# Optimization experiments

Measured on AMD Instinct MI355X. Metric: run time of the kernel, lower is better.

## Reference

```python
import jax, jax.numpy as jnp
import numpy as np

NUM_NODES = 100000
NUM_EDGES = 1600000
IN_DIM, HID_DIM, OUT_DIM = 128, 128, 70


def gcn_conv(x, edge_index, W, b):
    """PyG-style GCNConv: linear transform, add self-loops, symmetric
    degree-normalized scatter-add aggregation, plus bias."""
    n = x.shape[0]
    xw = x @ W  # [N, D_out]
    src, dst = edge_index[0], edge_index[1]  # messages flow src -> dst
    loop = jnp.arange(n)
    src = jnp.concatenate([src, loop])
    dst = jnp.concatenate([dst, loop])
    # degree computed at target nodes (with self-loops), edge weight 1
    deg = jax.ops.segment_sum(jnp.ones_like(dst, dtype=xw.dtype), dst,
                              num_segments=n)
    dinv = jnp.where(deg > 0, jax.lax.rsqrt(deg), 0.0)
    norm = dinv[src] * dinv[dst]  # [E+N]
    msgs = xw[src] * norm[:, None]  # [E+N, D_out] gathered messages
    out = jax.ops.segment_sum(msgs, dst, num_segments=n)
    return out + b


def setup_inputs() -> dict:
    key = jax.random.key(0)
    k = jax.random.split(key, 6)
    x = jax.random.normal(k[0], (NUM_NODES, IN_DIM), dtype=jnp.float32)
    edge_index = jax.random.randint(k[1], (2, NUM_EDGES), 0, NUM_NODES,
                                    dtype=jnp.int64)
    # Glorot-style init for weights, zero bias (PyG default)
    W1 = jax.random.normal(k[2], (IN_DIM, HID_DIM), dtype=jnp.float32) / np.sqrt(IN_DIM)
    b1 = jnp.zeros((HID_DIM,), dtype=jnp.float32)
    W2 = jax.random.normal(k[3], (HID_DIM, OUT_DIM), dtype=jnp.float32) / np.sqrt(HID_DIM)
    b2 = jnp.zeros((OUT_DIM,), dtype=jnp.float32)
    return {"x": x, "edge_index": edge_index, "W1": W1, "b1": b1,
            "W2": W2, "b2": b2}


def reference(x, edge_index, W1, b1, W2, b2):
    h = gcn_conv(x, edge_index, W1, b1)
    h = jax.nn.relu(h)
    # dropout(p=0.5) is identity in eval mode
    out = gcn_conv(h, edge_index, W2, b2)
    return out
```

## Files before the change

### kernel.cpp

```cpp
#include <hip/hip_runtime.h>
#include <hip/hip_bf16.h>


#define BSH 8
#define BCHUNK 4096
#define BCAP 8192

typedef __attribute__((ext_vector_type(8))) short short8;
typedef __attribute__((ext_vector_type(4))) float float4v;
typedef __attribute__((ext_vector_type(2))) float float2v;

__device__ __forceinline__ float bf_lo(unsigned u) { return __uint_as_float(u << 16); }
__device__ __forceinline__ float bf_hi(unsigned u) { return __uint_as_float(u & 0xffff0000u); }
__device__ __forceinline__ float bf2f(unsigned short h) {
    return __uint_as_float((unsigned)h << 16);
}
__device__ __forceinline__ unsigned short f2bf(float f) {
    unsigned u = __float_as_uint(f);
    u += 0x7fff + ((u >> 16) & 1);
    return (unsigned short)(u >> 16);
}
__device__ __forceinline__ void acc8(float* acc, uint4 m) {
    acc[0] += bf_lo(m.x); acc[1] += bf_hi(m.x);
    acc[2] += bf_lo(m.y); acc[3] += bf_hi(m.y);
    acc[4] += bf_lo(m.z); acc[5] += bf_hi(m.z);
    acc[6] += bf_lo(m.w); acc[7] += bf_hi(m.w);
}

__global__ __launch_bounds__(512) void k_bucket_scatter(
        const int* __restrict__ src, const int* __restrict__ dst,
        int* __restrict__ bwcur, unsigned long long* __restrict__ tmp, int E, int nb) {
    __shared__ int lh[512];
    __shared__ int lb[512];
    int t = threadIdx.x;
    for (int j = t; j < nb; j += 512) lh[j] = 0;
    __syncthreads();
    int e0 = blockIdx.x * BCHUNK;
    int e1 = min(E, e0 + BCHUNK);
    for (int e = e0 + t; e < e1; e += 512) atomicAdd(&lh[dst[e] >> BSH], 1);
    __syncthreads();
    for (int j = t; j < nb; j += 512) {
        int c = lh[j];
        lb[j] = c ? atomicAdd(&bwcur[j], c) : 0;
        lh[j] = 0;
    }
    __syncthreads();
    for (int e = e0 + t; e < e1; e += 512) {
        int d = dst[e];
        int b = d >> BSH;
        int o = atomicAdd(&lh[b], 1);
        int pos = lb[b] + o;
        if (pos < BCAP)
            tmp[(size_t)b * BCAP + pos] =
                ((unsigned long long)(unsigned)d << 32) | (unsigned)src[e];
    }
}

__global__ __launch_bounds__(512) void k_bucket_finalize(
        const unsigned long long* __restrict__ tmp, const int* __restrict__ bwcur,
        int* __restrict__ deg, float* __restrict__ dinv,
        int* __restrict__ rs, int* __restrict__ csr, int N) {
    __shared__ int cnt[256];
    __shared__ int sc[256];
    int b = blockIdx.x;
    int t = threadIdx.x;
    int e0 = b * BCAP;
    int e1 = e0 + min(bwcur[b], BCAP);
    if (t < 256) cnt[t] = 0;
    __syncthreads();
    for (int e = e0 + t; e < e1; e += 512) {
        int d = (int)(tmp[e] >> 32);
        atomicAdd(&cnt[d & 255], 1);
    }
    __syncthreads();
    int c = (t < 256) ? cnt[t] : 0;
    if (t < 256) sc[t] = c;
    __syncthreads();
    for (int off = 1; off < 256; off <<= 1) {
        int add = (t >= off && t < 256) ? sc[t - off] : 0;
        __syncthreads();
        if (t < 256) sc[t] += add;
        __syncthreads();
    }
    int excl = (t < 256) ? (sc[t] - c) : 0;
    __syncthreads();
    if (t < 256) sc[t] = excl;
    int node = (b << BSH) + t;
    if (t < 256 && node < N) {
        deg[node] = c;
        dinv[node] = rsqrtf((float)(c + 1));
        rs[node] = e0 + excl;
    }
    if (t < 256) cnt[t] = 0;
    __syncthreads();
    for (int e = e0 + t; e < e1; e += 512) {
        unsigned long long p = tmp[e];
        int j = ((int)(p >> 32)) & 255;
        int o = atomicAdd(&cnt[j], 1);
        csr[e0 + sc[j] + o] = (int)(p & 0xffffffffu);
    }
}

__global__ void k_prep_w(const float* __restrict__ W1, const float* __restrict__ W2,
                         unsigned short* __restrict__ w1th, unsigned short* __restrict__ w1tl,
                         unsigned short* __restrict__ w2th, unsigned short* __restrict__ w2tl,
                         int* __restrict__ bwcur) {
    if (blockIdx.x >= 104) {
        int idx = (blockIdx.x - 104) * 256 + threadIdx.x;
        if (idx < 512) bwcur[idx] = 0;
        return;
    }
    int i = blockIdx.x * blockDim.x + threadIdx.x;
    if (i < 128 * 128) {
        int col = i % 128, k = i / 128;
        float w = W1[k * 128 + col];
        unsigned short h = f2bf(w);
        w1th[(size_t)col * 128 + k] = h;
        w1tl[(size_t)col * 128 + k] = f2bf(w - bf2f(h));
    } else if (i < 128 * 128 + 80 * 128) {
        int j = i - 128 * 128;
        int col = j % 80, k = j / 80;
        float w = (col < 70) ? W2[k * 70 + col] : 0.f;
        unsigned short h = f2bf(w);
        w2th[(size_t)col * 128 + k] = h;
        w2tl[(size_t)col * 128 + k] = f2bf(w - bf2f(h));
    }
}

template <int DOUT, int OSTRIDE, int NT>
__global__ __launch_bounds__(256, 3) void k_gemm_mfma(
        const float* __restrict__ X, const unsigned short* __restrict__ Wth,
        const unsigned short* __restrict__ Wtl,
        const float* __restrict__ dinv, unsigned short* __restrict__ Y, int n) {
    __shared__ short xs_h[64][136];
    __shared__ short xs_l[64][136];
    int t = threadIdx.x;
    int lane = t & 63, wave = t >> 6;
    int m16 = lane & 15, quad = lane >> 4;
    int r0 = blockIdx.x * 64;

    short8 bh[2][4], bl[2][4];
    int nt0 = wave, nt1 = wave + 4;
#pragma unroll
    for (int i = 0; i < 2; i++) {
        int nt = i ? nt1 : nt0;
        if (nt >= NT) continue;
        int col = nt * 16 + m16;
#pragma unroll
        for (int kc = 0; kc < 4; kc++) {
            bh[i][kc] = *(const short8*)&Wth[(size_t)col * 128 + kc * 32 + quad * 8];
            bl[i][kc] = *(const short8*)&Wtl[(size_t)col * 128 + kc * 32 + quad * 8];
        }
    }

    for (int p = t; p < 64 * 32; p += 256) {
        int row = p >> 5;
        int k4 = p & 31;
        int gr = r0 + row;
        if (gr >= n) gr = n - 1;
        float4v xv = __builtin_nontemporal_load(
            (const float4v*)(X + (size_t)gr * 128 + 4 * k4));
        unsigned short h0 = f2bf(xv.x), h1 = f2bf(xv.y);
        unsigned short h2 = f2bf(xv.z), h3 = f2bf(xv.w);
        unsigned short l0 = f2bf(xv.x - bf2f(h0)), l1 = f2bf(xv.y - bf2f(h1));
        unsigned short l2 = f2bf(xv.z - bf2f(h2)), l3 = f2bf(xv.w - bf2f(h3));
        *(uint2*)&xs_h[row][4 * k4] =
            make_uint2((unsigned)h0 | ((unsigned)h1 << 16), (unsigned)h2 | ((unsigned)h3 << 16));
        *(uint2*)&xs_l[row][4 * k4] =
            make_uint2((unsigned)l0 | ((unsigned)l1 << 16), (unsigned)l2 | ((unsigned)l3 << 16));
    }
    __syncthreads();

    float4v acc[2][4];
#pragma unroll
    for (int i = 0; i < 2; i++)
#pragma unroll
        for (int ms = 0; ms < 4; ms++) acc[i][ms] = (float4v){0.f, 0.f, 0.f, 0.f};

#pragma unroll
    for (int kc = 0; kc < 4; kc++) {
#pragma unroll
        for (int ms = 0; ms < 4; ms++) {
            short8 ah = *(short8*)&xs_h[ms * 16 + m16][kc * 32 + quad * 8];
            short8 al = *(short8*)&xs_l[ms * 16 + m16][kc * 32 + quad * 8];
#pragma unroll
            for (int i = 0; i < 2; i++) {
                int nt = i ? nt1 : nt0;
                if (nt >= NT) continue;
                acc[i][ms] = __builtin_amdgcn_mfma_f32_16x16x32_bf16(ah, bh[i][kc], acc[i][ms], 0, 0, 0);
                acc[i][ms] = __builtin_amdgcn_mfma_f32_16x16x32_bf16(al, bh[i][kc], acc[i][ms], 0, 0, 0);
                acc[i][ms] = __builtin_amdgcn_mfma_f32_16x16x32_bf16(ah, bl[i][kc], acc[i][ms], 0, 0, 0);
            }
        }
    }

#pragma unroll
    for (int i = 0; i < 2; i++) {
        int nt = i ? nt1 : nt0;
        if (nt >= NT) continue;
        int col = nt * 16 + m16;
        if (col >= OSTRIDE) continue;
#pragma unroll
        for (int ms = 0; ms < 4; ms++) {
#pragma unroll
            for (int r = 0; r < 4; r++) {
                int row = r0 + ms * 16 + quad * 4 + r;
                if (row < n) {
                    float val = (col < DOUT) ? acc[i][ms][r] * dinv[row] : 0.f;
                    Y[(size_t)row * OSTRIDE + col] = f2bf(val);
                }
            }
        }
    }
}

__global__ __launch_bounds__(256, 8) void k_agg_w128(
        const uint4* __restrict__ msg, const float* __restrict__ dinv,
        const int* __restrict__ rs, const int* __restrict__ deg,
        const int* __restrict__ csr, const float* __restrict__ bias,
        float* __restrict__ out, int n) {
    int lane = threadIdx.x & 63;
    int q = lane & 15;
    int slot = lane >> 4;
    int wid = blockIdx.x * 4 + (threadIdx.x >> 6);
    int nw = gridDim.x * 4;
    for (int v = wid; v < n; v += nw) {
        int start = rs[v];
        int cnt = deg[v];
        float dv = dinv[v];
        uint4 mself = msg[(size_t)v * 16 + q];
        float acc[8] = {0.f, 0.f, 0.f, 0.f, 0.f, 0.f, 0.f, 0.f};
        int i = slot;
        for (; i + 12 < cnt; i += 16) {
            int s0 = csr[start + i];
            int s1 = csr[start + i + 4];
            int s2 = csr[start + i + 8];
            int s3 = csr[start + i + 12];
            uint4 m0 = msg[(size_t)s0 * 16 + q];
            uint4 m1 = msg[(size_t)s1 * 16 + q];
            uint4 m2 = msg[(size_t)s2 * 16 + q];
            uint4 m3 = msg[(size_t)s3 * 16 + q];
            acc8(acc, m0);
            acc8(acc, m1);
            acc8(acc, m2);
            acc8(acc, m3);
        }
        for (; i + 4 < cnt; i += 8) {
            int s0 = csr[start + i];
            int s1 = csr[start + i + 4];
            uint4 m0 = msg[(size_t)s0 * 16 + q];
            uint4 m1 = msg[(size_t)s1 * 16 + q];
            acc8(acc, m0);
            acc8(acc, m1);
        }
        if (i < cnt) {
            int s = csr[start + i];
            uint4 m = msg[(size_t)s * 16 + q];
            acc8(acc, m);
        }
#pragma unroll
        for (int j = 0; j < 8; j++) acc[j] += __shfl_xor(acc[j], 32);
#pragma unroll
        for (int j = 0; j < 8; j++) acc[j] += __shfl_xor(acc[j], 16);
        if (slot == 0) {
            float o[8];
            o[0] = acc[0] + bf_lo(mself.x); o[1] = acc[1] + bf_hi(mself.x);
            o[2] = acc[2] + bf_lo(mself.y); o[3] = acc[3] + bf_hi(mself.y);
            o[4] = acc[4] + bf_lo(mself.z); o[5] = acc[5] + bf_hi(mself.z);
            o[6] = acc[6] + bf_lo(mself.w); o[7] = acc[7] + bf_hi(mself.w);
            float r[8];
#pragma unroll
            for (int j = 0; j < 8; j++) r[j] = fmaxf(dv * o[j] + bias[8 * q + j], 0.f);
            float4v* op = (float4v*)(out + (size_t)v * 128 + 8 * q);
            __builtin_nontemporal_store((float4v){r[0], r[1], r[2], r[3]}, op);
            __builtin_nontemporal_store((float4v){r[4], r[5], r[6], r[7]}, op + 1);
        }
    }
}

__global__ __launch_bounds__(256, 8) void k_agg_w72(
        const uint4* __restrict__ msg, const float* __restrict__ dinv,
        const int* __restrict__ rs, const int* __restrict__ deg,
        const int* __restrict__ csr, const float* __restrict__ bias,
        float* __restrict__ out, int n) {
    int lane = threadIdx.x & 63;
    int slot = lane / 9;
    int q = lane - slot * 9;
    bool active = lane < 63;
    int wid = blockIdx.x * 4 + (threadIdx.x >> 6);
    int nw = gridDim.x * 4;
    for (int v = wid; v < n; v += nw) {
        int start = rs[v];
        int cnt = deg[v];
        float dv = dinv[v];
        float acc[8] = {0.f, 0.f, 0.f, 0.f, 0.f, 0.f, 0.f, 0.f};
        uint4 mself = make_uint4(0, 0, 0, 0);
        if (active) {
            mself = msg[(size_t)v * 9 + q];
            int i = slot;
            for (; i + 14 < cnt; i += 21) {
                int s0 = csr[start + i];
                int s1 = csr[start + i + 7];
                int s2 = csr[start + i + 14];
                uint4 m0 = msg[(size_t)s0 * 9 + q];
                uint4 m1 = msg[(size_t)s1 * 9 + q];
                uint4 m2 = msg[(size_t)s2 * 9 + q];
                acc8(acc, m0);
                acc8(acc, m1);
                acc8(acc, m2);
            }
            for (; i + 7 < cnt; i += 14) {
                int s0 = csr[start + i];
                int s1 = csr[start + i + 7];
                uint4 m0 = msg[(size_t)s0 * 9 + q];
                uint4 m1 = msg[(size_t)s1 * 9 + q];
                acc8(acc, m0);
                acc8(acc, m1);
            }
            if (i < cnt) {
                int s = csr[start + i];
                uint4 m = msg[(size_t)s * 9 + q];
                acc8(acc, m);
            }
        }
#pragma unroll
        for (int j = 0; j < 8; j++) {
            float t27 = __shfl(acc[j], lane + 27);
            if (lane < 27) acc[j] += t27;
        }
#pragma unroll
        for (int j = 0; j < 8; j++) {
            float t54 = __shfl(acc[j], lane + 54);
            float t9  = __shfl(acc[j], lane + 9);
            float t18 = __shfl(acc[j], lane + 18);
            if (lane < 9) acc[j] += t54 + t9 + t18;
        }
        if (lane < 9) {
            float o[8];
            o[0] = acc[0] + bf_lo(mself.x); o[1] = acc[1] + bf_hi(mself.x);
            o[2] = acc[2] + bf_lo(mself.y); o[3] = acc[3] + bf_hi(mself.y);
            o[4] = acc[4] + bf_lo(mself.z); o[5] = acc[5] + bf_hi(mself.z);
            o[6] = acc[6] + bf_lo(mself.w); o[7] = acc[7] + bf_hi(mself.w);
            float* orow = out + (size_t)v * 70 + 8 * q;
#pragma unroll
            for (int jj = 0; jj < 4; jj++) {
                int f = 8 * q + 2 * jj;
                if (f < 70) {
                    float2 st = make_float2(dv * o[2 * jj] + bias[f],
                                            dv * o[2 * jj + 1] + bias[f + 1]);
                    *(float2*)(orow + 2 * jj) = st;
                }
            }
        }
    }
}

static inline size_t alignup(size_t x) { return (x + 255) & ~(size_t)255; }

extern "C" void kernel_launch(void* const* d_in, const int* in_sizes, int n_in,
                              void* d_out, int out_size, void* d_ws, size_t ws_size,
                              hipStream_t stream) {
    const float* x = (const float*)d_in[0];
    const int* edge = (const int*)d_in[1];
    const float* W1 = (const float*)d_in[2];
    const float* b1 = (const float*)d_in[3];
    const float* W2 = (const float*)d_in[4];
    const float* b2 = (const float*)d_in[5];

    const int N = in_sizes[0] / 128;
    const int E = in_sizes[1] / 2;
    const int* src = edge;
    const int* dst = edge + E;
    const int nb = (N + 255) >> BSH;

    char* w = (char*)d_ws;
    int* deg = (int*)w;              w += alignup((size_t)N * 4);
    float* dinv = (float*)w;         w += alignup((size_t)N * 4);
    int* rs = (int*)w;               w += alignup((size_t)N * 4);
    int* bwcur = (int*)w;            w += alignup(4096);
    int* csr = (int*)w;              w += alignup((size_t)nb * BCAP * 4);
    unsigned short* msg1 = (unsigned short*)w; w += alignup((size_t)N * 128 * 2);
    unsigned short* msg2 = (unsigned short*)w; w += alignup((size_t)N * 72 * 2);
    unsigned short* w1th = (unsigned short*)w; w += alignup(128 * 128 * 2);
    unsigned short* w1tl = (unsigned short*)w; w += alignup(128 * 128 * 2);
    unsigned short* w2th = (unsigned short*)w; w += alignup(80 * 128 * 2);
    unsigned short* w2tl = (unsigned short*)w; w += alignup(80 * 128 * 2);
    float* h = (float*)w;            w += alignup((size_t)N * 128 * 4);
    unsigned long long* tmp = (unsigned long long*)h;

    k_prep_w<<<104 + 2, 256, 0, stream>>>(W1, W2, w1th, w1tl, w2th, w2tl, bwcur);

    k_bucket_scatter<<<(E + BCHUNK - 1) / BCHUNK, 512, 0, stream>>>(src, dst, bwcur, tmp, E, nb);
    k_bucket_finalize<<<nb, 512, 0, stream>>>(tmp, bwcur, deg, dinv, rs, csr, N);

    int gblocks = (N + 63) / 64;

    k_gemm_mfma<128, 128, 8><<<gblocks, 256, 0, stream>>>(x, w1th, w1tl, dinv, msg1, N);
    k_agg_w128<<<2048, 256, 0, stream>>>((const uint4*)msg1, dinv, rs, deg, csr, b1, h, N);

    k_gemm_mfma<70, 72, 5><<<gblocks, 256, 0, stream>>>(h, w2th, w2tl, dinv, msg2, N);
    k_agg_w72<<<2048, 256, 0, stream>>>((const uint4*)msg2, dinv, rs, deg, csr, b2,
                                        (float*)d_out, N);
}
```

Before: 329.1 us.

## Split layer-2 messages into 64-wide main and 8-wide tail arrays

The second GEMM now writes its 72-column bf16 output as two arrays: a 64-column block with 128-byte rows and a separate 8-column tail with 16-byte rows. The layer-2 aggregation is rewritten to use 8 lanes per edge across 8 edge slots, with a 4-way unrolled gather. One lane per slot also gathers the tail entry, and the reduction becomes simple xor shuffles. The goal is to cut the cache lines touched per gathered neighbour compared with the old 144-byte rows, and to remove the awkward 9-lane grouping. The cost is an extra scattered tail load per edge and a divergent branch on one lane per slot.

```diff
diff --git a/kernel.cpp b/kernel.cpp
--- a/kernel.cpp
+++ b/kernel.cpp
@@ -127,7 +127,7 @@
     }
 }
 
-template <int DOUT, int OSTRIDE, int NT>
+template <int DOUT, int OSTRIDE, int NT, int MODE>
 __global__ __launch_bounds__(256, 3) void k_gemm_mfma(
         const float* __restrict__ X, const unsigned short* __restrict__ Wth,
         const unsigned short* __restrict__ Wtl,
@@ -199,7 +199,7 @@
         int nt = i ? nt1 : nt0;
         if (nt >= NT) continue;
         int col = nt * 16 + m16;
-        if (col >= OSTRIDE) continue;
+        if (MODE == 0 && col >= OSTRIDE) continue;
 #pragma unroll
         for (int ms = 0; ms < 4; ms++) {
 #pragma unroll
@@ -207,7 +207,14 @@
                 int row = r0 + ms * 16 + quad * 4 + r;
                 if (row < n) {
                     float val = (col < DOUT) ? acc[i][ms][r] * dinv[row] : 0.f;
-                    Y[(size_t)row * OSTRIDE + col] = f2bf(val);
+                    if (MODE == 0) {
+                        Y[(size_t)row * OSTRIDE + col] = f2bf(val);
+                    } else {
+                        if (col < 64)
+                            Y[(size_t)row * 64 + col] = f2bf(val);
+                        else if (col < 72)
+                            Y[(size_t)n * 64 + (size_t)row * 8 + (col - 64)] = f2bf(val);
+                    }
                 }
             }
         }
@@ -278,15 +285,16 @@
     }
 }
 
-__global__ __launch_bounds__(256, 8) void k_agg_w72(
-        const uint4* __restrict__ msg, const float* __restrict__ dinv,
+__global__ __launch_bounds__(256, 8) void k_agg_w64b(
+        const uint4* __restrict__ msgA, const uint4* __restrict__ msgB,
+        const float* __restrict__ dinv,
         const int* __restrict__ rs, const int* __restrict__ deg,
         const int* __restrict__ csr, const float* __restrict__ bias,
         float* __restrict__ out, int n) {
     int lane = threadIdx.x & 63;
-    int slot = lane / 9;
-    int q = lane - slot * 9;
-    bool active = lane < 63;
+    int q = lane & 7;
+    int slot = lane >> 3;
+    bool bq = (q == 0);
     int wid = blockIdx.x * 4 + (threadIdx.x >> 6);
     int nw = gridDim.x * 4;
     for (int v = wid; v < n; v += nw) {
@@ -294,61 +302,83 @@
         int cnt = deg[v];
         float dv = dinv[v];
         float acc[8] = {0.f, 0.f, 0.f, 0.f, 0.f, 0.f, 0.f, 0.f};
-        uint4 mself = make_uint4(0, 0, 0, 0);
-        if (active) {
-            mself = msg[(size_t)v * 9 + q];
-            int i = slot;
-            for (; i + 14 < cnt; i += 21) {
-                int s0 = csr[start + i];
-                int s1 = csr[start + i + 7];
-                int s2 = csr[start + i + 14];
-                uint4 m0 = msg[(size_t)s0 * 9 + q];
-                uint4 m1 = msg[(size_t)s1 * 9 + q];
-                uint4 m2 = msg[(size_t)s2 * 9 + q];
-                acc8(acc, m0);
-                acc8(acc, m1);
-                acc8(acc, m2);
-            }
-            for (; i + 7 < cnt; i += 14) {
-                int s0 = csr[start + i];
-                int s1 = csr[start + i + 7];
-                uint4 m0 = msg[(size_t)s0 * 9 + q];
-                uint4 m1 = msg[(size_t)s1 * 9 + q];
-                acc8(acc, m0);
-                acc8(acc, m1);
-            }
-            if (i < cnt) {
-                int s = csr[start + i];
-                uint4 m = msg[(size_t)s * 9 + q];
-                acc8(acc, m);
+        float bacc[6] = {0.f, 0.f, 0.f, 0.f, 0.f, 0.f};
+        int i = slot;
+        for (; i + 24 < cnt; i += 32) {
+            int s0 = csr[start + i];
+            int s1 = csr[start + i + 8];
+            int s2 = csr[start + i + 16];
+            int s3 = csr[start + i + 24];
+            uint4 a0 = msgA[(size_t)s0 * 8 + q];
+            uint4 a1 = msgA[(size_t)s1 * 8 + q];
+            uint4 a2 = msgA[(size_t)s2 * 8 + q];
+            uint4 a3 = msgA[(size_t)s3 * 8 + q];
+            acc8(acc, a0);
+            acc8(acc, a1);
+            acc8(acc, a2);
+            acc8(acc, a3);
+            if (bq) {
+                uint4 b0 = msgB[s0];
+                uint4 b1 = msgB[s1];
+                uint4 b2_ = msgB[s2];
+                uint4 b3 = msgB[s3];
+                bacc[0] += bf_lo(b0.x) + bf_lo(b1.x) + bf_lo(b2_.x) + bf_lo(b3.x);
+                bacc[1] += bf_hi(b0.x) + bf_hi(b1.x) + bf_hi(b2_.x) + bf_hi(b3.x);
+                bacc[2] += bf_lo(b0.y) + bf_lo(b1.y) + bf_lo(b2_.y) + bf_lo(b3.y);
+                bacc[3] += bf_hi(b0.y) + bf_hi(b1.y) + bf_hi(b2_.y) + bf_hi(b3.y);
+                bacc[4] += bf_lo(b0.z) + bf_lo(b1.z) + bf_lo(b2_.z) + bf_lo(b3.z);
+                bacc[5] += bf_hi(b0.z) + bf_hi(b1.z) + bf_hi(b2_.z) + bf_hi(b3.z);
+            }
+        }
+        for (; i < cnt; i += 8) {
+            int s = csr[start + i];
+            uint4 a = msgA[(size_t)s * 8 + q];
+            acc8(acc, a);
+            if (bq) {
+                uint4 b0 = msgB[s];
+                bacc[0] += bf_lo(b0.x); bacc[1] += bf_hi(b0.x);
+                bacc[2] += bf_lo(b0.y); bacc[3] += bf_hi(b0.y);
+                bacc[4] += bf_lo(b0.z); bacc[5] += bf_hi(b0.z);
             }
         }
 #pragma unroll
         for (int j = 0; j < 8; j++) {
-            float t27 = __shfl(acc[j], lane + 27);
-            if (lane < 27) acc[j] += t27;
-        }
-#pragma unroll
-        for (int j = 0; j < 8; j++) {
-            float t54 = __shfl(acc[j], lane + 54);
-            float t9  = __shfl(acc[j], lane + 9);
-            float t18 = __shfl(acc[j], lane + 18);
-            if (lane < 9) acc[j] += t54 + t9 + t18;
-        }
-        if (lane < 9) {
+            acc[j] += __shfl_xor(acc[j], 8);
+            acc[j] += __shfl_xor(acc[j], 16);
+            acc[j] += __shfl_xor(acc[j], 32);
+        }
+#pragma unroll
+        for (int j = 0; j < 6; j++) {
+            bacc[j] += __shfl_xor(bacc[j], 8);
+            bacc[j] += __shfl_xor(bacc[j], 16);
+            bacc[j] += __shfl_xor(bacc[j], 32);
+        }
+        if (slot == 0) {
+            uint4 aself = msgA[(size_t)v * 8 + q];
             float o[8];
-            o[0] = acc[0] + bf_lo(mself.x); o[1] = acc[1] + bf_hi(mself.x);
-            o[2] = acc[2] + bf_lo(mself.y); o[3] = acc[3] + bf_hi(mself.y);
-            o[4] = acc[4] + bf_lo(mself.z); o[5] = acc[5] + bf_hi(mself.z);
-            o[6] = acc[6] + bf_lo(mself.w); o[7] = acc[7] + bf_hi(mself.w);
+            o[0] = acc[0] + bf_lo(aself.x); o[1] = acc[1] + bf_hi(aself.x);
+            o[2] = acc[2] + bf_lo(aself.y); o[3] = acc[3] + bf_hi(aself.y);
+            o[4] = acc[4] + bf_lo(aself.z); o[5] = acc[5] + bf_hi(aself.z);
+            o[6] = acc[6] + bf_lo(aself.w); o[7] = acc[7] + bf_hi(aself.w);
             float* orow = out + (size_t)v * 70 + 8 * q;
 #pragma unroll
             for (int jj = 0; jj < 4; jj++) {
-                int f = 8 * q + 2 * jj;
-                if (f < 70) {
-                    float2 st = make_float2(dv * o[2 * jj] + bias[f],
-                                            dv * o[2 * jj + 1] + bias[f + 1]);
-                    *(float2*)(orow + 2 * jj) = st;
+                float2 st = make_float2(dv * o[2 * jj] + bias[8 * q + 2 * jj],
+                                        dv * o[2 * jj + 1] + bias[8 * q + 2 * jj + 1]);
+                *(float2*)(orow + 2 * jj) = st;
+            }
+            if (q == 0) {
+                uint4 bself = msgB[v];
+                float bo[6];
+                bo[0] = bacc[0] + bf_lo(bself.x); bo[1] = bacc[1] + bf_hi(bself.x);
+                bo[2] = bacc[2] + bf_lo(bself.y); bo[3] = bacc[3] + bf_hi(bself.y);
+                bo[4] = bacc[4] + bf_lo(bself.z); bo[5] = bacc[5] + bf_hi(bself.z);
+                float* brow = out + (size_t)v * 70 + 64;
+#pragma unroll
+                for (int jj = 0; jj < 3; jj++) {
+                    float2 st = make_float2(dv * bo[2 * jj] + bias[64 + 2 * jj],
+                                            dv * bo[2 * jj + 1] + bias[64 + 2 * jj + 1]);
+                    *(float2*)(brow + 2 * jj) = st;
                 }
             }
         }
@@ -395,10 +425,11 @@
 
     int gblocks = (N + 63) / 64;
 
-    k_gemm_mfma<128, 128, 8><<<gblocks, 256, 0, stream>>>(x, w1th, w1tl, dinv, msg1, N);
+    k_gemm_mfma<128, 128, 8, 0><<<gblocks, 256, 0, stream>>>(x, w1th, w1tl, dinv, msg1, N);
     k_agg_w128<<<2048, 256, 0, stream>>>((const uint4*)msg1, dinv, rs, deg, csr, b1, h, N);
 
-    k_gemm_mfma<70, 72, 5><<<gblocks, 256, 0, stream>>>(h, w2th, w2tl, dinv, msg2, N);
-    k_agg_w72<<<2048, 256, 0, stream>>>((const uint4*)msg2, dinv, rs, deg, csr, b2,
-                                        (float*)d_out, N);
-}
+    k_gemm_mfma<70, 72, 5, 2><<<gblocks, 256, 0, stream>>>(h, w2th, w2tl, dinv, msg2, N);
+    k_agg_w64b<<<2048, 256, 0, stream>>>(
+        (const uint4*)msg2, (const uint4*)(msg2 + (size_t)N * 64), dinv, rs, deg, csr,
+        b2, (float*)d_out, N);
+}
```

After: 347.3 us. 1.06x slower.
